# Kernel tuning notes

Hardware: AMD Instinct MI355X
Metric: run time of the kernel (lower is better)

The kernel has to match this reference:

```python
import jax, jax.numpy as jnp
import numpy as np

N = 100000      # number of 1-simplices (edges of the power grid)
NNZ = 3200000   # nonzeros in L1_tilde (avg degree 32)
CIN = 128
COUT = 128
BN_EPS = 1e-5


def setup_inputs() -> dict:
    key = jax.random.key(0)
    ks = jax.random.split(key, 8)
    Z_H = jax.random.normal(ks[0], (N, CIN), dtype=jnp.float32)
    rows = jax.random.randint(ks[1], (NNZ,), 0, N)
    cols = jax.random.randint(ks[2], (NNZ,), 0, N)
    values = jax.random.normal(ks[3], (NNZ,), dtype=jnp.float32)
    # nn.Linear params (Kaiming-ish scale)
    W = jax.random.normal(ks[4], (CIN, COUT), dtype=jnp.float32) / np.float32(np.sqrt(CIN))
    b = jnp.zeros((COUT,), dtype=jnp.float32)
    # BatchNorm1d affine params
    gamma = jnp.ones((COUT,), dtype=jnp.float32)
    beta = jnp.zeros((COUT,), dtype=jnp.float32)
    return {"Z_H": Z_H, "values": values, "W": W, "b": b,
            "gamma": gamma, "beta": beta, "rows": rows, "cols": cols}


def reference(Z_H, values, W, b, gamma, beta, rows, cols):
    # Linear projection: [N, CIN] @ [CIN, COUT] + [COUT]
    Z_theta = Z_H @ W + b
    # Sparse Laplacian matmul (COO SpMM): Z_conv[r] += v * Z_theta[c]
    gathered = values[:, None] * Z_theta[cols]          # [NNZ, COUT]
    Z_conv = jax.ops.segment_sum(gathered, rows, num_segments=Z_H.shape[0])
    # BatchNorm1d (training mode: biased batch stats over the node dim)
    mean = jnp.mean(Z_conv, axis=0)
    var = jnp.var(Z_conv, axis=0)
    Z_bn = (Z_conv - mean) * (gamma / jnp.sqrt(var + BN_EPS)) + beta
    # ReLU + row-wise max pool -> [N, 1]
    Z_psi = jax.nn.relu(Z_bn)
    return jnp.max(Z_psi, axis=1, keepdims=True)
```

## Files before the change

kernel.cpp:

```cpp
#include <hip/hip_runtime.h>
#include <hip/hip_bf16.h>

#define CIN  128
#define COUT 128
#define BN_EPS 1e-5f
#define RPB   64
#define MAXNB 2048
#define PCHUNK 8192
#define CAP   2560
#define LDP   136

typedef __attribute__((ext_vector_type(8))) short short8;
typedef __attribute__((ext_vector_type(4))) float f32x4;

__device__ __forceinline__ unsigned pk2bf(float lo, float hi) {
    union { __hip_bfloat162 h; unsigned u; } c;
    c.h = __float22bfloat162_rn(make_float2(lo, hi));
    return c.u;
}

__device__ __forceinline__ void gemm_body(
    const float* __restrict__ Z, const float* __restrict__ W,
    const float* __restrict__ b, unsigned short* __restrict__ Zt,
    int N, int bid, int gb)
{
    __shared__ unsigned short cls[64 * LDP];

    const int t    = threadIdx.x;
    const int lane = t & 63;
    const int wid  = t >> 6;
    const int lm   = lane & 15;
    const int lg   = lane >> 4;

    short8 bfr[4][8];
#pragma unroll
    for (int kc = 0; kc < 4; ++kc) {
#pragma unroll
        for (int ct = 0; ct < 8; ++ct) {
            union { short8 v; unsigned u32[4]; } bf;
#pragma unroll
            for (int e = 0; e < 8; e += 2) {
                const float w0 = W[(kc * 32 + lg * 8 + e)     * COUT + ct * 16 + lm];
                const float w1 = W[(kc * 32 + lg * 8 + e + 1) * COUT + ct * 16 + lm];
                bf.u32[e >> 1] = pk2bf(w0, w1);
            }
            bfr[kc][ct] = bf.v;
        }
    }

    float bias[8];
#pragma unroll
    for (int ct = 0; ct < 8; ++ct) bias[ct] = b[ct * 16 + lm];

    const int tr = t >> 4;
    const int cc = t & 15;

    const int ntiles = (N + 63) / 64;
    for (int tile = bid; tile < ntiles; tile += gb) {
        const int row0 = tile * 64 + wid * 16;
        const int arow = row0 + lm;
        const bool aval = arow < N;
        const float* zrow = Z + (size_t)arow * CIN;

        f32x4 acc[8];
#pragma unroll
        for (int ct = 0; ct < 8; ++ct) {
            f32x4 a = {bias[ct], bias[ct], bias[ct], bias[ct]};
            acc[ct] = a;
        }

#pragma unroll
        for (int kc = 0; kc < 4; ++kc) {
            union { short8 v; unsigned u32[4]; } af;
            if (aval) {
                const float4 z0 = *((const float4*)(zrow + kc * 32 + lg * 8));
                const float4 z1 = *((const float4*)(zrow + kc * 32 + lg * 8 + 4));
                af.u32[0] = pk2bf(z0.x, z0.y);
                af.u32[1] = pk2bf(z0.z, z0.w);
                af.u32[2] = pk2bf(z1.x, z1.y);
                af.u32[3] = pk2bf(z1.z, z1.w);
            } else {
#pragma unroll
                for (int e = 0; e < 4; ++e) af.u32[e] = 0;
            }
#pragma unroll
            for (int ct = 0; ct < 8; ++ct)
                acc[ct] = __builtin_amdgcn_mfma_f32_16x16x32_bf16(
                    af.v, bfr[kc][ct], acc[ct], 0, 0, 0);
        }

        __syncthreads();
#pragma unroll
        for (int i = 0; i < 4; ++i) {
            const int r = wid * 16 + lg * 4 + i;
#pragma unroll
            for (int ct = 0; ct < 8; ct += 2) {
                const unsigned u = pk2bf(acc[ct][i], acc[ct + 1][i]);
                cls[r * LDP + ct * 16 + lm]       = (unsigned short)(u & 0xffffu);
                cls[r * LDP + (ct + 1) * 16 + lm] = (unsigned short)(u >> 16);
            }
        }
        __syncthreads();

#pragma unroll
        for (int j = 0; j < 4; ++j) {
            const int r = j * 16 + tr;
            const int grow = tile * 64 + r;
            if (grow < N) {
                const uint4 v = *((const uint4*)&cls[r * LDP + cc * 8]);
                *((uint4*)(Zt + (size_t)grow * COUT + cc * 8)) = v;
            }
        }
    }
}

__device__ __forceinline__ void partition_body(
    const int* __restrict__ rows, const int* __restrict__ cols,
    const float* __restrict__ vals, int* __restrict__ bucketCur,
    uint2* __restrict__ ebuck, int nnz, int NB, int pb)
{
    __shared__ int h[MAXNB];
    __shared__ int basecur[MAXNB];
    const int t = threadIdx.x;

    for (int i = t; i < NB; i += 256) h[i] = 0;
    __syncthreads();

    const int c0 = pb * PCHUNK;
    const int ce = min(c0 + PCHUNK, nnz);

    int rloc[PCHUNK / 256];
#pragma unroll
    for (int j = 0; j < PCHUNK / 256; ++j) {
        const int i = c0 + j * 256 + t;
        int r = -1;
        if (i < ce) r = rows[i];
        rloc[j] = r;
        if (r >= 0) atomicAdd(&h[r >> 6], 1);
    }
    __syncthreads();

    for (int i = t; i < NB; i += 256) {
        const int c = h[i];
        basecur[i] = c ? (i * CAP + atomicAdd(&bucketCur[i], c)) : 0;
    }
    __syncthreads();

#pragma unroll
    for (int j = 0; j < PCHUNK / 256; ++j) {
        const int i = c0 + j * 256 + t;
        const int r = rloc[j];
        if (r >= 0) {
            const int p = atomicAdd(&basecur[r >> 6], 1);
            ebuck[p] = make_uint2((unsigned)cols[i] | ((unsigned)(r & (RPB - 1)) << 17),
                                  __float_as_uint(vals[i]));
        }
    }
}

__global__ __launch_bounds__(256, 2) void gemm_part_kernel(
    const float* __restrict__ Z, const float* __restrict__ W,
    const float* __restrict__ b, unsigned short* __restrict__ Zt,
    const int* __restrict__ rows, const int* __restrict__ cols,
    const float* __restrict__ vals, int* __restrict__ bucketCur,
    uint2* __restrict__ ebuck, int nnz, int N, int NB, int pblocks, int gb)
{
    if ((int)blockIdx.x < pblocks) {
        partition_body(rows, cols, vals, bucketCur, ebuck, nnz, NB, blockIdx.x);
    } else {
        gemm_body(Z, W, b, Zt, N, blockIdx.x - pblocks, gb);
    }
}

__global__ __launch_bounds__(256) void gather_build_kernel(
    const unsigned short* __restrict__ Zt, const uint2* __restrict__ ebuck,
    const int* __restrict__ bucketCur, unsigned int* __restrict__ Zc,
    float* __restrict__ stats, int N)
{
    __shared__ int cnt[RPB];
    __shared__ int scn[RPB];
    __shared__ int loc[RPB];
    __shared__ uint2 ebuf[CAP];
    __shared__ float sbuf[256];

    const int t = threadIdx.x;
    const int b = blockIdx.x;
    const int base = b * CAP;
    int count = bucketCur[b];
    if (count > CAP) count = CAP;

    sbuf[t] = 0.f;
    if (t < RPB) cnt[t] = 0;
    __syncthreads();

    uint2 er[CAP / 256];
#pragma unroll
    for (int j = 0; j < CAP / 256; ++j) {
        const int i = j * 256 + t;
        if (i < count) {
            er[j] = ebuck[base + i];
            atomicAdd(&cnt[er[j].x >> 17], 1);
        }
    }
    __syncthreads();

    if (t < RPB) scn[t] = cnt[t];
    __syncthreads();
#pragma unroll
    for (int off = 1; off < RPB; off <<= 1) {
        int v = 0;
        if (t < RPB && t >= off) v = scn[t - off];
        __syncthreads();
        if (t < RPB) scn[t] += v;
        __syncthreads();
    }
    if (t < RPB) loc[t] = scn[t] - cnt[t];
    __syncthreads();

#pragma unroll
    for (int j = 0; j < CAP / 256; ++j) {
        const int i = j * 256 + t;
        if (i < count) {
            const uint2 e = er[j];
            const int rl  = (int)(e.x >> 17);
            const int pos = atomicAdd(&loc[rl], 1);
            ebuf[pos] = make_uint2(e.x & 0x1FFFFu, e.y);
        }
    }
    __syncthreads();

    const int wid  = t >> 6;
    const int lane = t & 63;
    const int eo   = lane >> 5;
    const int cg   = lane & 31;

    const int row0 = b * RPB;

#pragma unroll
    for (int pass = 0; pass < 2; ++pass) {
        const int choff = pass * 64 + cg * 2;

        float s0 = 0.f, s1 = 0.f, q0 = 0.f, q1 = 0.f;

        for (int r = wid; r < RPB; r += 4) {
            const int row = row0 + r;
            if (row >= N) break;
            const int end = scn[r];
            const int beg = end - cnt[r];

            float a0 = 0.f, a1 = 0.f;

            int i = beg + eo;
            for (; i + 6 < end; i += 8) {
                const uint2 p0 = ebuf[i];
                const uint2 p1 = ebuf[i + 2];
                const uint2 p2 = ebuf[i + 4];
                const uint2 p3 = ebuf[i + 6];
                const unsigned g0 = *((const unsigned*)(Zt + (size_t)p0.x * COUT + choff));
                const unsigned g1 = *((const unsigned*)(Zt + (size_t)p1.x * COUT + choff));
                const unsigned g2 = *((const unsigned*)(Zt + (size_t)p2.x * COUT + choff));
                const unsigned g3 = *((const unsigned*)(Zt + (size_t)p3.x * COUT + choff));
                const float v0 = __uint_as_float(p0.y);
                const float v1 = __uint_as_float(p1.y);
                const float v2 = __uint_as_float(p2.y);
                const float v3 = __uint_as_float(p3.y);
                a0 = fmaf(v0, __uint_as_float(g0 << 16), a0);
                a1 = fmaf(v0, __uint_as_float(g0 & 0xffff0000u), a1);
                a0 = fmaf(v1, __uint_as_float(g1 << 16), a0);
                a1 = fmaf(v1, __uint_as_float(g1 & 0xffff0000u), a1);
                a0 = fmaf(v2, __uint_as_float(g2 << 16), a0);
                a1 = fmaf(v2, __uint_as_float(g2 & 0xffff0000u), a1);
                a0 = fmaf(v3, __uint_as_float(g3 << 16), a0);
                a1 = fmaf(v3, __uint_as_float(g3 & 0xffff0000u), a1);
            }
            for (; i < end; i += 2) {
                const uint2 p = ebuf[i];
                const unsigned g = *((const unsigned*)(Zt + (size_t)p.x * COUT + choff));
                const float vp = __uint_as_float(p.y);
                a0 = fmaf(vp, __uint_as_float(g << 16), a0);
                a1 = fmaf(vp, __uint_as_float(g & 0xffff0000u), a1);
            }

            a0 += __shfl_xor(a0, 32);
            a1 += __shfl_xor(a1, 32);

            if (eo == 0) {
                Zc[(size_t)row * (COUT / 2) + pass * 32 + cg] = pk2bf(a0, a1);
                s0 += a0; s1 += a1;
                q0 = fmaf(a0, a0, q0);
                q1 = fmaf(a1, a1, q1);
            }
        }

        if (eo == 0) {
            atomicAdd(&sbuf[choff + 0], s0);
            atomicAdd(&sbuf[choff + 1], s1);
            atomicAdd(&sbuf[128 + choff + 0], q0);
            atomicAdd(&sbuf[128 + choff + 1], q1);
        }
    }
    __syncthreads();
    atomicAdd(&stats[t], sbuf[t]);
}

__global__ __launch_bounds__(256) void finalize_kernel(
    const unsigned int* __restrict__ Zc, const float* __restrict__ stats,
    const float* __restrict__ gamma, const float* __restrict__ beta,
    float* __restrict__ out, int N)
{
    const int row = blockIdx.x * 4 + (threadIdx.x >> 6);
    if (row >= N) return;
    const int lane = threadIdx.x & 63;
    const int c0 = lane * 2;

    const unsigned g = Zc[(size_t)row * (COUT / 2) + lane];
    const float x0 = __uint_as_float(g << 16);
    const float x1 = __uint_as_float(g & 0xffff0000u);

    const float invN = 1.0f / (float)N;
    const float m0 = stats[c0] * invN;
    const float m1 = stats[c0 + 1] * invN;
    const float v0 = stats[128 + c0] * invN - m0 * m0;
    const float v1 = stats[128 + c0 + 1] * invN - m1 * m1;
    const float sc0 = gamma[c0]     * rsqrtf(v0 + BN_EPS);
    const float sc1 = gamma[c0 + 1] * rsqrtf(v1 + BN_EPS);

    float y0 = (x0 - m0) * sc0 + beta[c0];
    float y1 = (x1 - m1) * sc1 + beta[c0 + 1];
    y0 = fmaxf(y0, 0.f);
    y1 = fmaxf(y1, 0.f);

    float mx = fmaxf(y0, y1);
#pragma unroll
    for (int off = 32; off > 0; off >>= 1)
        mx = fmaxf(mx, __shfl_xor(mx, off));

    if (lane == 0) out[row] = mx;
}

extern "C" void kernel_launch(void* const* d_in, const int* in_sizes, int n_in,
                              void* d_out, int out_size, void* d_ws, size_t ws_size,
                              hipStream_t stream)
{
    const float* Z_H   = (const float*)d_in[0];
    const float* vals  = (const float*)d_in[1];
    const float* W     = (const float*)d_in[2];
    const float* b     = (const float*)d_in[3];
    const float* gamma = (const float*)d_in[4];
    const float* beta  = (const float*)d_in[5];
    const int*   rows  = (const int*)d_in[6];
    const int*   cols  = (const int*)d_in[7];
    float* out = (float*)d_out;

    const int N   = in_sizes[0] / CIN;
    const int nnz = in_sizes[1];
    const int NB  = (N + RPB - 1) / RPB;
    const int pblocks = (nnz + PCHUNK - 1) / PCHUNK;
    const int ntiles  = (N + 63) / 64;
    const int gb      = (ntiles + 2) / 3;

    char* ws = (char*)d_ws;
    size_t off = 0;
    unsigned short* Zt = (unsigned short*)(ws + off); off += (size_t)N * COUT * sizeof(unsigned short);
    unsigned int*   Zc = (unsigned int*)(ws + off);   off += (size_t)N * (COUT / 2) * sizeof(unsigned int);
    uint2* ebuck  = (uint2*)(ws + off);  off += (size_t)NB * CAP * sizeof(uint2);
    int* bucketCur = (int*)(ws + off);   off += (size_t)NB * sizeof(int);
    float* stats   = (float*)(ws + off); off += 256 * sizeof(float);

    hipMemsetAsync(bucketCur, 0, ((size_t)NB + 256) * sizeof(int), stream);

    gemm_part_kernel<<<pblocks + gb, 256, 0, stream>>>(
        Z_H, W, b, Zt, rows, cols, vals, bucketCur, ebuck, nnz, N, NB, pblocks, gb);

    gather_build_kernel<<<NB, 256, 0, stream>>>(Zt, ebuck, bucketCur, Zc, stats, N);

    finalize_kernel<<<(N + 3) / 4, 256, 0, stream>>>(Zc, stats, gamma, beta, out, N);
}
```

Baseline: 232.7 us.

## Stage bf16 weights in shared LDS instead of registers, raise occupancy

The GEMM body now converts W to bf16 once per block into LDS, laid out in MFMA fragment order, and reads the B fragments from LDS per k-chunk instead of keeping all 32 short8 fragments in registers. Shared memory for the partition and GEMM paths is merged into one union buffer, launch bounds go from 2 to 3 blocks per SIMD set, and the GEMM grid shrinks to a quarter of the tiles. The goal is to cut VGPR pressure so more waves fit and the fused partition/GEMM kernel hides memory latency better. The cost is extra LDS reads on every MFMA, a larger 49 KB LDS footprint per block, and fewer GEMM blocks each doing more tiles.

```diff
diff --git a/kernel.cpp b/kernel.cpp
--- a/kernel.cpp
+++ b/kernel.cpp
@@ -9,6 +9,7 @@
 #define PCHUNK 8192
 #define CAP   2560
 #define LDP   136
+#define SMEM_BYTES 50176
 
 typedef __attribute__((ext_vector_type(8))) short short8;
 typedef __attribute__((ext_vector_type(4))) float f32x4;
@@ -22,9 +23,10 @@
 __device__ __forceinline__ void gemm_body(
     const float* __restrict__ Z, const float* __restrict__ W,
     const float* __restrict__ b, unsigned short* __restrict__ Zt,
-    int N, int bid, int gb)
-{
-    __shared__ unsigned short cls[64 * LDP];
+    int N, int bid, int gb, char* smem)
+{
+    unsigned*       Wlds = (unsigned*)smem;
+    unsigned short* cls  = (unsigned short*)(smem + 32768);
 
     const int t    = threadIdx.x;
     const int lane = t & 63;
@@ -32,25 +34,24 @@
     const int lm   = lane & 15;
     const int lg   = lane >> 4;
 
-    short8 bfr[4][8];
-#pragma unroll
-    for (int kc = 0; kc < 4; ++kc) {
-#pragma unroll
-        for (int ct = 0; ct < 8; ++ct) {
-            union { short8 v; unsigned u32[4]; } bf;
-#pragma unroll
-            for (int e = 0; e < 8; e += 2) {
-                const float w0 = W[(kc * 32 + lg * 8 + e)     * COUT + ct * 16 + lm];
-                const float w1 = W[(kc * 32 + lg * 8 + e + 1) * COUT + ct * 16 + lm];
-                bf.u32[e >> 1] = pk2bf(w0, w1);
-            }
-            bfr[kc][ct] = bf.v;
-        }
+#pragma unroll
+    for (int j = 0; j < 32; ++j) {
+        const int i  = j * 256 + t;
+        const int k2 = i >> 7;
+        const int c  = i & 127;
+        const float w0 = W[(k2 * 2)     * COUT + c];
+        const float w1 = W[(k2 * 2 + 1) * COUT + c];
+        const int k  = k2 * 2;
+        const int kc = k >> 5;
+        const int lgs = (k >> 3) & 3;
+        const int s  = (k & 7) >> 1;
+        Wlds[(((kc * 8 + (c >> 4)) * 64) + lgs * 16 + (c & 15)) * 4 + s] = pk2bf(w0, w1);
     }
 
     float bias[8];
 #pragma unroll
     for (int ct = 0; ct < 8; ++ct) bias[ct] = b[ct * 16 + lm];
+    __syncthreads();
 
     const int tr = t >> 4;
     const int cc = t & 15;
@@ -84,9 +85,10 @@
                 for (int e = 0; e < 4; ++e) af.u32[e] = 0;
             }
 #pragma unroll
-            for (int ct = 0; ct < 8; ++ct)
-                acc[ct] = __builtin_amdgcn_mfma_f32_16x16x32_bf16(
-                    af.v, bfr[kc][ct], acc[ct], 0, 0, 0);
+            for (int ct = 0; ct < 8; ++ct) {
+                const short8 bf = *((const short8*)(Wlds + ((kc * 8 + ct) * 64 + lane) * 4));
+                acc[ct] = __builtin_amdgcn_mfma_f32_16x16x32_bf16(af.v, bf, acc[ct], 0, 0, 0);
+            }
         }
 
         __syncthreads();
@@ -117,10 +119,10 @@
 __device__ __forceinline__ void partition_body(
     const int* __restrict__ rows, const int* __restrict__ cols,
     const float* __restrict__ vals, int* __restrict__ bucketCur,
-    uint2* __restrict__ ebuck, int nnz, int NB, int pb)
-{
-    __shared__ int h[MAXNB];
-    __shared__ int basecur[MAXNB];
+    uint2* __restrict__ ebuck, int nnz, int NB, int pb, char* smem)
+{
+    int* h       = (int*)smem;
+    int* basecur = h + MAXNB;
     const int t = threadIdx.x;
 
     for (int i = t; i < NB; i += 256) h[i] = 0;
@@ -158,17 +160,18 @@
     }
 }
 
-__global__ __launch_bounds__(256, 2) void gemm_part_kernel(
+__global__ __launch_bounds__(256, 3) void gemm_part_kernel(
     const float* __restrict__ Z, const float* __restrict__ W,
     const float* __restrict__ b, unsigned short* __restrict__ Zt,
     const int* __restrict__ rows, const int* __restrict__ cols,
     const float* __restrict__ vals, int* __restrict__ bucketCur,
     uint2* __restrict__ ebuck, int nnz, int N, int NB, int pblocks, int gb)
 {
+    __shared__ char smem[SMEM_BYTES];
     if ((int)blockIdx.x < pblocks) {
-        partition_body(rows, cols, vals, bucketCur, ebuck, nnz, NB, blockIdx.x);
+        partition_body(rows, cols, vals, bucketCur, ebuck, nnz, NB, blockIdx.x, smem);
     } else {
-        gemm_body(Z, W, b, Zt, N, blockIdx.x - pblocks, gb);
+        gemm_body(Z, W, b, Zt, N, blockIdx.x - pblocks, gb, smem);
     }
 }
 
@@ -357,7 +360,7 @@
     const int NB  = (N + RPB - 1) / RPB;
     const int pblocks = (nnz + PCHUNK - 1) / PCHUNK;
     const int ntiles  = (N + 63) / 64;
-    const int gb      = (ntiles + 2) / 3;
+    const int gb      = (ntiles + 3) / 4;
 
     char* ws = (char*)d_ws;
     size_t off = 0;
```

Measured after the change: 229.4 us. Within noise of the previous version (-1.4%).
